# Kernel tuning notes

Hardware: AMD Instinct MI355X
Metric: run time of the kernel (lower is better)

The kernel has to match this reference:

```python
import jax, jax.numpy as jnp
import numpy as np

N_SAM, N_GEN, N_E = 10000, 20000, 1000000
D_SAM, D_GEN = 2000, 500
D0, H = 256, [256, 128, 64]
SLOPE = 0.25


def _glorot(key, shape):
    fan_in, fan_out = shape
    s = jnp.sqrt(2.0 / (fan_in + fan_out))
    return jax.random.normal(key, shape, dtype=jnp.float32) * s


def setup_inputs() -> dict:
    key = jax.random.key(0)
    ks = jax.random.split(key, 24)
    inp = {
        "sam_feat": jax.random.normal(ks[0], (N_SAM, D_SAM), dtype=jnp.float32),
        "gen_feat": jax.random.normal(ks[1], (N_GEN, D_GEN), dtype=jnp.float32),
        "src_sg": jax.random.randint(ks[2], (N_E,), 0, N_SAM, dtype=jnp.int32),
        "dst_sg": jax.random.randint(ks[3], (N_E,), 0, N_GEN, dtype=jnp.int32),
        "src_gs": jax.random.randint(ks[4], (N_E,), 0, N_GEN, dtype=jnp.int32),
        "dst_gs": jax.random.randint(ks[5], (N_E,), 0, N_SAM, dtype=jnp.int32),
        # input projections (LinearLayer, xavier init)
        "l1_W": _glorot(ks[6], (D_SAM, D0)), "l1_b": jnp.zeros((D0,), jnp.float32),
        "l2_W": _glorot(ks[7], (D_GEN, D0)), "l2_b": jnp.zeros((D0,), jnp.float32),
    }
    dims = [(D0, H[0]), (H[0], H[1]), (H[1], H[2])]
    k = 8
    for i, (di, do) in enumerate(dims, start=1):
        for rel in ("sg", "gs"):
            inp[f"W{i}_{rel}"] = _glorot(ks[k], (di, do)); k += 1
            inp[f"b{i}_{rel}"] = jnp.zeros((do,), jnp.float32)
    return inp


def _graph_conv(h_src, src, dst, n_src, n_dst, W, b):
    """DGL GraphConv with norm='both': D_dst^{-1/2} A D_src^{-1/2} h W + b."""
    ones = jnp.ones(src.shape, dtype=h_src.dtype)
    deg_out = jnp.clip(jax.ops.segment_sum(ones, src, num_segments=n_src), 1.0)
    deg_in = jnp.clip(jax.ops.segment_sum(ones, dst, num_segments=n_dst), 1.0)
    h = h_src * jax.lax.rsqrt(deg_out)[:, None]
    agg = jax.ops.segment_sum(h[src], dst, num_segments=n_dst)  # [n_dst, d]
    agg = agg * jax.lax.rsqrt(deg_in)[:, None]
    return agg @ W + b


def reference(sam_feat, gen_feat, src_sg, dst_sg, src_gs, dst_gs,
              l1_W, l1_b, l2_W, l2_b,
              W1_sg, b1_sg, W1_gs, b1_gs,
              W2_sg, b2_sg, W2_gs, b2_gs,
              W3_sg, b3_sg, W3_gs, b3_gs):
    h_sam = sam_feat @ l1_W + l1_b
    h_gen = gen_feat @ l2_W + l2_b
    layers = [(W1_sg, b1_sg, W1_gs, b1_gs),
              (W2_sg, b2_sg, W2_gs, b2_gs),
              (W3_sg, b3_sg, W3_gs, b3_gs)]
    for Wsg, bsg, Wgs, bgs in layers:
        # HeteroGraphConv(sum): dst 'gen' receives from sam_gen, dst 'sam' from gen_sam
        new_gen = _graph_conv(h_sam, src_sg, dst_sg, N_SAM, N_GEN, Wsg, bsg)
        new_sam = _graph_conv(h_gen, src_gs, dst_gs, N_GEN, N_SAM, Wgs, bgs)
        h_sam = jax.nn.leaky_relu(new_sam, SLOPE)  # dropout is identity in eval mode
        h_gen = jax.nn.leaky_relu(new_gen, SLOPE)
    return h_sam, h_gen
```

## Files before the change

### kernel.cpp

```cpp
#include <hip/hip_runtime.h>
#include <hip/hip_bf16.h>
#include <stdint.h>

#define N_SAM 10000
#define N_GEN 20000
#define DSAM  2000
#define DGEN  500
#define NB    32
#define NBNS  10240
#define SSPAN 2560
#define MP_SAM 10048
#define MP_GEN 20032

typedef __hip_bfloat16 bf16;
typedef short bf16x8 __attribute__((ext_vector_type(8)));
typedef float f32x4 __attribute__((ext_vector_type(4)));
typedef float f32x2 __attribute__((ext_vector_type(2)));

__device__ __forceinline__ float bfbits2f(unsigned short u) {
    unsigned v = ((unsigned)u) << 16;
    return __builtin_bit_cast(float, v);
}
__device__ __forceinline__ unsigned short f2bfbits(float f) {
    bf16 h = __float2bfloat16(f);
    return __builtin_bit_cast(unsigned short, h);
}
__device__ __forceinline__ unsigned packbf2(float lo, float hi) {
    return ((unsigned)f2bfbits(lo)) | (((unsigned)f2bfbits(hi)) << 16);
}
__device__ __forceinline__ f32x2 b2f2(unsigned x) {
    f32x2 r;
    r.x = __builtin_bit_cast(float, x << 16);
    r.y = __builtin_bit_cast(float, x & 0xffff0000u);
    return r;
}
__device__ __forceinline__ void addu2(uint4 u, f32x2* a) {
    a[0] += b2f2(u.x);
    a[1] += b2f2(u.y);
    a[2] += b2f2(u.z);
    a[3] += b2f2(u.w);
}
__device__ __forceinline__ void gload16(const unsigned short* g, unsigned short* l) {
    __builtin_amdgcn_global_load_lds(
        (const __attribute__((address_space(1))) void*)g,
        (__attribute__((address_space(3))) void*)l, 16, 0, 0);
}

__global__ __launch_bounds__(1024) void hist_count_kernel(
    const int* __restrict__ ssg, const int* __restrict__ dsg,
    const int* __restrict__ sgs, const int* __restrict__ dgs,
    unsigned* __restrict__ cs_ssg, unsigned* __restrict__ cs_dsg,
    unsigned* __restrict__ cs_sgs, unsigned* __restrict__ cs_dgs,
    int ne, int chunk) {
    __shared__ unsigned bins[NBNS];
    const int* arr; unsigned* counts; int lo, hi, nb;
    switch (blockIdx.y) {
        case 0:  arr = ssg; counts = cs_ssg; lo = 0;     hi = 10000; nb = 10000; break;
        case 1:  arr = dsg; counts = cs_dsg; lo = 0;     hi = 10240; nb = 20000; break;
        case 2:  arr = dsg; counts = cs_dsg; lo = 10240; hi = 20000; nb = 20000; break;
        case 3:  arr = sgs; counts = cs_sgs; lo = 0;     hi = 10240; nb = 20000; break;
        case 4:  arr = sgs; counts = cs_sgs; lo = 10240; hi = 20000; nb = 20000; break;
        default: arr = dgs; counts = cs_dgs; lo = 0;     hi = 10000; nb = 10000; break;
    }
    int span = hi - lo;
    for (int i = threadIdx.x; i < span; i += 1024) bins[i] = 0u;
    __syncthreads();
    int blk = blockIdx.x;
    int e0 = blk * chunk;
    int e1 = e0 + chunk; if (e1 > ne) e1 = ne;
    for (int e = e0 + threadIdx.x; e < e1; e += 1024) {
        int b = arr[e];
        if (b >= lo && b < hi) atomicAdd(&bins[b - lo], 1u);
    }
    __syncthreads();
    unsigned* out = counts + (size_t)blk * nb + lo;
    for (int i = threadIdx.x; i < span; i += 1024) out[i] = bins[i];
}

__global__ __launch_bounds__(256) void reduce_counts_kernel(
    const unsigned* __restrict__ cs_ssg, const unsigned* __restrict__ cs_dsg,
    const unsigned* __restrict__ cs_sgs, const unsigned* __restrict__ cs_dgs,
    unsigned* __restrict__ cnt_dsg, unsigned* __restrict__ cnt_dgs,
    float* __restrict__ rs_out_sam, float* __restrict__ rs_in_gen,
    float* __restrict__ rs_out_gen, float* __restrict__ rs_in_sam) {
    int i = blockIdx.x * 256 + threadIdx.x;
    int which = blockIdx.y;
    const unsigned* cs; int nb;
    switch (which) {
        case 0:  cs = cs_ssg; nb = 10000; break;
        case 1:  cs = cs_dsg; nb = 20000; break;
        case 2:  cs = cs_sgs; nb = 20000; break;
        default: cs = cs_dgs; nb = 10000; break;
    }
    if (i >= nb) return;
    unsigned s = 0;
    #pragma unroll 4
    for (int b = 0; b < NB; b++) s += cs[(size_t)b * nb + i];
    unsigned c = (s < 1u) ? 1u : s;
    float r = rsqrtf((float)c);
    if (which == 0)      { rs_out_sam[i] = r; }
    else if (which == 1) { cnt_dsg[i] = s; rs_in_gen[i] = r; }
    else if (which == 2) { rs_out_gen[i] = r; }
    else                 { cnt_dgs[i] = s; rs_in_sam[i] = r; }
}

__global__ __launch_bounds__(1024) void scan2_kernel(
    const unsigned* __restrict__ c0, unsigned* __restrict__ r0, int nA,
    const unsigned* __restrict__ c1, unsigned* __restrict__ r1, int nB) {
    const unsigned* cnt; unsigned* row; int n;
    if (blockIdx.x == 0) { cnt = c0; row = r0; n = nA; }
    else                 { cnt = c1; row = r1; n = nB; }
    __shared__ unsigned sdata[1024];
    __shared__ unsigned carry_s;
    int t = threadIdx.x;
    if (t == 0) carry_s = 0;
    __syncthreads();
    for (int base = 0; base < n; base += 1024) {
        int i = base + t;
        unsigned v = (i < n) ? cnt[i] : 0u;
        sdata[t] = v;
        __syncthreads();
        for (int off = 1; off < 1024; off <<= 1) {
            unsigned add = (t >= off) ? sdata[t - off] : 0u;
            __syncthreads();
            sdata[t] += add;
            __syncthreads();
        }
        unsigned incl = sdata[t];
        unsigned carry = carry_s;
        if (i < n) row[i] = carry + incl - v;
        __syncthreads();
        if (t == 1023) carry_s = carry + incl;
        __syncthreads();
    }
    if (t == 0) row[n] = carry_s;
}

__global__ __launch_bounds__(256) void cursor_kernel(
    const unsigned* __restrict__ cs_dsg, const unsigned* __restrict__ cs_dgs,
    const unsigned* __restrict__ row_sg, const unsigned* __restrict__ row_gs,
    unsigned* __restrict__ cur_sg_m, unsigned* __restrict__ cur_gs_m) {
    int i = blockIdx.x * 256 + threadIdx.x;
    const unsigned* cs; const unsigned* row; unsigned* cur; int nb;
    if (blockIdx.y == 0) { cs = cs_dsg; row = row_sg; cur = cur_sg_m; nb = 20000; }
    else                 { cs = cs_dgs; row = row_gs; cur = cur_gs_m; nb = 10000; }
    if (i >= nb) return;
    unsigned run = row[i];
    for (int b = 0; b < NB; b++) {
        cur[(size_t)b * nb + i] = run;
        run += cs[(size_t)b * nb + i];
    }
}

__global__ __launch_bounds__(1024) void scatter_sorted_kernel(
    const int* __restrict__ src_sg, const int* __restrict__ dst_sg,
    const int* __restrict__ src_gs, const int* __restrict__ dst_gs,
    const unsigned* __restrict__ cur_sg_m, const unsigned* __restrict__ cur_gs_m,
    int* __restrict__ col_sg, int* __restrict__ col_gs, int ne, int chunk) {
    __shared__ unsigned curs[SSPAN];
    int sl = blockIdx.y;
    const int* src; const int* dst; const unsigned* cmat; int* col; int lo, hi, nb;
    if (sl < 8) {
        src = src_sg; dst = dst_sg; cmat = cur_sg_m; col = col_sg; nb = 20000;
        lo = sl * SSPAN; hi = lo + SSPAN; if (hi > 20000) hi = 20000;
    } else {
        src = src_gs; dst = dst_gs; cmat = cur_gs_m; col = col_gs; nb = 10000;
        lo = (sl - 8) * SSPAN; hi = lo + SSPAN; if (hi > 10000) hi = 10000;
    }
    int span = hi - lo, blk = blockIdx.x;
    const unsigned* cin = cmat + (size_t)blk * nb + lo;
    for (int i = threadIdx.x; i < span; i += 1024) curs[i] = cin[i];
    __syncthreads();
    int e0 = blk * chunk;
    int e1 = e0 + chunk; if (e1 > ne) e1 = ne;
    for (int e = e0 + threadIdx.x; e < e1; e += 1024) {
        int d = dst[e];
        if (d >= lo && d < hi) {
            unsigned p = atomicAdd(&curs[d - lo], 1u);
            col[p] = src[e];
        }
    }
}

__global__ __launch_bounds__(256) void convert_feat_kernel(
    const float* __restrict__ src, unsigned short* __restrict__ dst,
    int M, int K, int Mp, int kshift) {
    const int Kp = 1 << kshift;
    size_t ng = ((size_t)Mp << kshift) >> 3;
    for (size_t gi = (size_t)blockIdx.x * 256 + threadIdx.x; gi < ng;
         gi += (size_t)gridDim.x * 256) {
        size_t o8 = gi << 3;
        int row = (int)(o8 >> kshift);
        int col = (int)(o8 & (size_t)(Kp - 1));
        uint4 out;
        if (row < M && col + 8 <= K) {
            const float* p = src + (size_t)row * K + col;
            float4 u0 = *reinterpret_cast<const float4*>(p);
            float4 u1 = *reinterpret_cast<const float4*>(p + 4);
            out.x = packbf2(u0.x, u0.y);
            out.y = packbf2(u0.z, u0.w);
            out.z = packbf2(u1.x, u1.y);
            out.w = packbf2(u1.z, u1.w);
        } else {
            unsigned short v[8];
            #pragma unroll
            for (int j = 0; j < 8; j++) {
                float f = 0.0f;
                if (row < M && col + j < K) f = src[(size_t)row * K + col + j];
                v[j] = f2bfbits(f);
            }
            out.x = ((unsigned)v[0]) | (((unsigned)v[1]) << 16);
            out.y = ((unsigned)v[2]) | (((unsigned)v[3]) << 16);
            out.z = ((unsigned)v[4]) | (((unsigned)v[5]) << 16);
            out.w = ((unsigned)v[6]) | (((unsigned)v[7]) << 16);
        }
        *reinterpret_cast<uint4*>(dst + o8) = out;
    }
}

__global__ __launch_bounds__(256) void zero_pad_kernel(
    unsigned short* __restrict__ p0, int n0,
    unsigned short* __restrict__ p1, int n1) {
    int i = blockIdx.x * 256 + threadIdx.x;
    if (i < n0) p0[i] = 0;
    if (i < n1) p1[i] = 0;
}

struct WDesc { const float* src; unsigned short* dst; int K, N, Kp; };
struct WPack { WDesc d[8]; };

__global__ __launch_bounds__(256) void transpose_weights_kernel(WPack p) {
    WDesc d = p.d[blockIdx.z];
    int n  = blockIdx.x * 32 + threadIdx.x;
    int kp = blockIdx.y * 8 + threadIdx.y;
    if (n >= d.N || kp >= d.Kp) return;
    float v = (kp < d.K) ? d.src[(size_t)kp * d.N + n] : 0.0f;
    d.dst[(size_t)n * d.Kp + kp] = f2bfbits(v);
}

struct GemmDesc {
    const unsigned short* A; const unsigned short* BT;
    const float* bias; const float* rs; unsigned short* C;
    int M, N, Kp, GX, GY;
};

__global__ __launch_bounds__(256) void gemm2_bf16(GemmDesc da, GemmDesc db, int nblkA) {
    int bi = blockIdx.x;
    GemmDesc d;
    if (bi < nblkA) { d = da; } else { d = db; bi -= nblkA; }
    int xcd = bi & 7, g = bi >> 3;
    int ntile = g % d.GX;
    int mtile = (g / d.GX) * 8 + xcd;
    if (mtile >= d.GY) return;
    int m0 = mtile * 64, n0 = ntile * 64;
    int Kp = d.Kp;

    __shared__ __attribute__((aligned(16))) unsigned short As[2][64 * 64];
    __shared__ __attribute__((aligned(16))) unsigned short Bs[2][64 * 64];

    int t = threadIdx.x;
    int lane = t & 63;
    int wave = t >> 6;
    int wm = (wave >> 1) * 32, wn = (wave & 1) * 32;
    int q = lane >> 4, mr = lane & 15;

    int r0 = t >> 3;
    int sw = ((t & 7) ^ (r0 & 7)) << 3;
    const unsigned short* a0 = d.A + (size_t)(m0 + r0) * Kp + sw;
    const unsigned short* b0 = d.BT + (size_t)(n0 + r0) * Kp + sw;
    const size_t rstep = (size_t)32 * Kp;
    unsigned short* asl0 = &As[0][t * 8];
    unsigned short* asl1 = &As[0][(256 + t) * 8];
    unsigned short* bsl0 = &Bs[0][t * 8];
    unsigned short* bsl1 = &Bs[0][(256 + t) * 8];
    const int bufoff = 64 * 64;

    f32x4 acc[2][2] = {};

    gload16(a0, asl0);
    gload16(a0 + rstep, asl1);
    gload16(b0, bsl0);
    gload16(b0 + rstep, bsl1);
    __syncthreads();

    int nt = Kp >> 6;
    for (int it = 0; it < nt; ++it) {
        int cur = it & 1;
        if (it + 1 < nt) {
            int k0 = (it + 1) << 6;
            int boff = (cur ^ 1) * bufoff;
            gload16(a0 + k0,         asl0 + boff);
            gload16(a0 + rstep + k0, asl1 + boff);
            gload16(b0 + k0,         bsl0 + boff);
            gload16(b0 + rstep + k0, bsl1 + boff);
        }
        #pragma unroll
        for (int kk = 0; kk < 64; kk += 32) {
            bf16x8 af[2], bfr[2];
            int cb = (kk >> 3) + q;
            #pragma unroll
            for (int i = 0; i < 2; i++) {
                int row = wm + i * 16 + mr;
                af[i] = *reinterpret_cast<const bf16x8*>(
                    &As[cur][row * 64 + ((cb ^ (row & 7)) << 3)]);
            }
            #pragma unroll
            for (int j = 0; j < 2; j++) {
                int row = wn + j * 16 + mr;
                bfr[j] = *reinterpret_cast<const bf16x8*>(
                    &Bs[cur][row * 64 + ((cb ^ (row & 7)) << 3)]);
            }
            #pragma unroll
            for (int i = 0; i < 2; i++)
                #pragma unroll
                for (int j = 0; j < 2; j++)
                    acc[i][j] = __builtin_amdgcn_mfma_f32_16x16x32_bf16(
                        af[i], bfr[j], acc[i][j], 0, 0, 0);
        }
        __syncthreads();
    }

    #pragma unroll
    for (int i = 0; i < 2; i++) {
        #pragma unroll
        for (int r = 0; r < 4; r++) {
            int row = m0 + wm + i * 16 + q * 4 + r;
            if (row >= d.M) continue;
            float sc = (d.rs != nullptr) ? d.rs[row] : 1.0f;
            #pragma unroll
            for (int j = 0; j < 2; j++) {
                int col = n0 + wn + j * 16 + mr;
                float v = acc[i][j][r];
                if (d.bias != nullptr) v += d.bias[col];
                v *= sc;
                d.C[(size_t)row * d.N + col] = f2bfbits(v);
            }
        }
    }
}

struct AggTask {
    const unsigned* rowptr; const int* col; const unsigned short* P;
    const float* rs_in; const float* bias; const float* rs_next;
    void* out;
    int row_begin; int row_end; int D; int d0; int lprs;
};
struct AggPack { AggTask t[8]; };

template <bool OUTBF>
__global__ __launch_bounds__(256) void agg_xcd_kernel(AggPack pk) {
    int task = blockIdx.x & 7;
    int lblk = blockIdx.x >> 3;
    int nlb  = (int)gridDim.x >> 3;
    AggTask t = pk.t[task];
    int lane = threadIdx.x & 63;
    int wav  = threadIdx.x >> 6;
    const int LPR = 1 << t.lprs;
    const int R   = 64 >> t.lprs;
    int sub = lane >> t.lprs;
    int li  = lane & (LPR - 1);
    const int D = t.D;
    const unsigned short* __restrict__ P = t.P + t.d0 + li * 8;
    const int* __restrict__ col = t.col;
    const int R4 = R << 2;

    for (int r = t.row_begin + lblk * 4 + wav; r < t.row_end; r += nlb * 4) {
        unsigned e0 = t.rowptr[r], e1 = t.rowptr[r + 1];
        f32x2 ac0[4] = {}, ac1[4] = {};
        unsigned e = e0;
        for (; e + (unsigned)R4 <= e1; e += R4) {
            int s0 = col[e + sub];
            int s1 = col[e + R + sub];
            int s2 = col[e + 2 * R + sub];
            int s3 = col[e + 3 * R + sub];
            uint4 u0 = *reinterpret_cast<const uint4*>(P + (size_t)s0 * D);
            uint4 u1 = *reinterpret_cast<const uint4*>(P + (size_t)s1 * D);
            uint4 u2 = *reinterpret_cast<const uint4*>(P + (size_t)s2 * D);
            uint4 u3 = *reinterpret_cast<const uint4*>(P + (size_t)s3 * D);
            addu2(u0, ac0); addu2(u1, ac1); addu2(u2, ac0); addu2(u3, ac1);
        }
        for (; e < e1; e += R) {
            unsigned idx = e + sub;
            if (idx < e1) {
                int s0 = col[idx];
                uint4 u = *reinterpret_cast<const uint4*>(P + (size_t)s0 * D);
                addu2(u, ac0);
            }
        }
        float acf[8];
        #pragma unroll
        for (int j = 0; j < 4; j++) {
            f32x2 s = ac0[j] + ac1[j];
            acf[2 * j]     = s.x;
            acf[2 * j + 1] = s.y;
        }
        for (int off = 32; off >= LPR; off >>= 1) {
            #pragma unroll
            for (int j = 0; j < 8; j++) acf[j] += __shfl_down(acf[j], off);
        }
        if (sub == 0) {
            float rsv = t.rs_in[r];
            float res[8];
            #pragma unroll
            for (int j = 0; j < 8; j++) {
                float v = acf[j] * rsv + t.bias[t.d0 + li * 8 + j];
                res[j] = (v >= 0.f) ? v : 0.25f * v;
            }
            if constexpr (OUTBF) {
                float sn = t.rs_next[r];
                uint4 o;
                o.x = packbf2(res[0] * sn, res[1] * sn);
                o.y = packbf2(res[2] * sn, res[3] * sn);
                o.z = packbf2(res[4] * sn, res[5] * sn);
                o.w = packbf2(res[6] * sn, res[7] * sn);
                *reinterpret_cast<uint4*>(
                    (unsigned short*)t.out + (size_t)r * D + t.d0 + li * 8) = o;
            } else {
                float* op = (float*)t.out + (size_t)r * D + t.d0 + li * 8;
                *reinterpret_cast<float4*>(op)     = make_float4(res[0], res[1], res[2], res[3]);
                *reinterpret_cast<float4*>(op + 4) = make_float4(res[4], res[5], res[6], res[7]);
            }
        }
    }
}

extern "C" void kernel_launch(void* const* d_in, const int* in_sizes, int n_in,
                              void* d_out, int out_size, void* d_ws, size_t ws_size,
                              hipStream_t stream) {
    const float* sam_feat = (const float*)d_in[0];
    const float* gen_feat = (const float*)d_in[1];
    const int* src_sg = (const int*)d_in[2];
    const int* dst_sg = (const int*)d_in[3];
    const int* src_gs = (const int*)d_in[4];
    const int* dst_gs = (const int*)d_in[5];
    const float* l1W = (const float*)d_in[6];
    const float* l1b = (const float*)d_in[7];
    const float* l2W = (const float*)d_in[8];
    const float* l2b = (const float*)d_in[9];
    const float* Wsg[3] = {(const float*)d_in[10], (const float*)d_in[14], (const float*)d_in[18]};
    const float* bsg[3] = {(const float*)d_in[11], (const float*)d_in[15], (const float*)d_in[19]};
    const float* Wgs[3] = {(const float*)d_in[12], (const float*)d_in[16], (const float*)d_in[20]};
    const float* bgs[3] = {(const float*)d_in[13], (const float*)d_in[17], (const float*)d_in[21]};
    const int NE = in_sizes[2];
    const int CHUNK = (NE + NB - 1) / NB;

    char* base = (char*)d_ws;
    size_t off = 0;
    auto alloc = [&](size_t bytes) -> char* {
        char* p = base + off;
        off = (off + bytes + 255) & ~(size_t)255;
        return p;
    };
    unsigned* cs_ssg = (unsigned*)alloc((size_t)NB * N_SAM * 4);
    unsigned* cs_dsg = (unsigned*)alloc((size_t)NB * N_GEN * 4);
    unsigned* cs_sgs = (unsigned*)alloc((size_t)NB * N_GEN * 4);
    unsigned* cs_dgs = (unsigned*)alloc((size_t)NB * N_SAM * 4);
    unsigned* cnt_dsg = (unsigned*)alloc(N_GEN * 4);
    unsigned* cnt_dgs = (unsigned*)alloc(N_SAM * 4);
    unsigned* row_sg = (unsigned*)alloc((N_GEN + 1) * 4);
    unsigned* row_gs = (unsigned*)alloc((N_SAM + 1) * 4);
    unsigned* cur_sg_m = (unsigned*)alloc((size_t)NB * N_GEN * 4);
    unsigned* cur_gs_m = (unsigned*)alloc((size_t)NB * N_SAM * 4);
    float* rs_out_sam = (float*)alloc(N_SAM * 4);
    float* rs_in_sam  = (float*)alloc(N_SAM * 4);
    float* rs_out_gen = (float*)alloc(N_GEN * 4);
    float* rs_in_gen  = (float*)alloc(N_GEN * 4);
    int* col_sg = (int*)alloc((size_t)NE * 4);
    int* col_gs = (int*)alloc((size_t)NE * 4);
    unsigned short* hs = (unsigned short*)alloc((size_t)MP_SAM * 256 * 2);
    unsigned short* hg = (unsigned short*)alloc((size_t)MP_GEN * 256 * 2);
    unsigned short* ps = (unsigned short*)alloc((size_t)N_SAM * 256 * 2);
    unsigned short* pg = (unsigned short*)alloc((size_t)N_GEN * 256 * 2);
    const int KP1 = 2048, KP2 = 512;
    unsigned short* BT_l1 = (unsigned short*)alloc((size_t)256 * KP1 * 2);
    unsigned short* BT_l2 = (unsigned short*)alloc((size_t)256 * KP2 * 2);
    unsigned short* BT_sg[3], *BT_gs[3];
    const int LN[3] = {256, 128, 64};
    const int LK[3] = {256, 256, 128};
    for (int i = 0; i < 3; i++) {
        BT_sg[i] = (unsigned short*)alloc((size_t)LN[i] * LK[i] * 2);
        BT_gs[i] = (unsigned short*)alloc((size_t)LN[i] * LK[i] * 2);
    }
    unsigned short* A_sam = (unsigned short*)alloc((size_t)MP_SAM * KP1 * 2);
    unsigned short* A_gen = (unsigned short*)alloc((size_t)MP_GEN * KP2 * 2);
    (void)ws_size;

    hist_count_kernel<<<dim3(NB, 6), 1024, 0, stream>>>(
        src_sg, dst_sg, src_gs, dst_gs, cs_ssg, cs_dsg, cs_sgs, cs_dgs, NE, CHUNK);
    reduce_counts_kernel<<<dim3((N_GEN + 255) / 256, 4), 256, 0, stream>>>(
        cs_ssg, cs_dsg, cs_sgs, cs_dgs, cnt_dsg, cnt_dgs,
        rs_out_sam, rs_in_gen, rs_out_gen, rs_in_sam);
    scan2_kernel<<<2, 1024, 0, stream>>>(cnt_dsg, row_sg, N_GEN, cnt_dgs, row_gs, N_SAM);
    cursor_kernel<<<dim3((N_GEN + 255) / 256, 2), 256, 0, stream>>>(
        cs_dsg, cs_dgs, row_sg, row_gs, cur_sg_m, cur_gs_m);
    scatter_sorted_kernel<<<dim3(NB, 12), 1024, 0, stream>>>(
        src_sg, dst_sg, src_gs, dst_gs, cur_sg_m, cur_gs_m, col_sg, col_gs, NE, CHUNK);

    convert_feat_kernel<<<2048, 256, 0, stream>>>(sam_feat, A_sam, N_SAM, DSAM, MP_SAM, 11);
    convert_feat_kernel<<<1024, 256, 0, stream>>>(gen_feat, A_gen, N_GEN, DGEN, MP_GEN, 9);
    zero_pad_kernel<<<48, 256, 0, stream>>>(
        hs + (size_t)N_SAM * 256, (MP_SAM - N_SAM) * 256,
        hg + (size_t)N_GEN * 256, (MP_GEN - N_GEN) * 256);

    WPack wp;
    wp.d[0] = {l1W,    BT_l1,    DSAM, 256, KP1};
    wp.d[1] = {l2W,    BT_l2,    DGEN, 256, KP2};
    wp.d[2] = {Wsg[0], BT_sg[0], 256, 256, 256};
    wp.d[3] = {Wgs[0], BT_gs[0], 256, 256, 256};
    wp.d[4] = {Wsg[1], BT_sg[1], 256, 128, 256};
    wp.d[5] = {Wgs[1], BT_gs[1], 256, 128, 256};
    wp.d[6] = {Wsg[2], BT_sg[2], 128, 64, 128};
    wp.d[7] = {Wgs[2], BT_gs[2], 128, 64, 128};
    transpose_weights_kernel<<<dim3(8, KP1 / 8, 8), dim3(32, 8), 0, stream>>>(wp);

    dim3 blk(256);
    const int GY_SAM = (N_SAM + 63) / 64;
    const int GY_GEN = (N_GEN + 63) / 64;
    auto swgrid = [](int GX, int GY) { return 8 * GX * ((GY + 7) / 8); };
    const int AGG_GRID = 2048;

    auto mkg = [](const unsigned short* A, const unsigned short* BT,
                  const float* bias, const float* rs, unsigned short* C,
                  int M, int N, int Kp, int GX, int GY) {
        GemmDesc d; d.A = A; d.BT = BT; d.bias = bias; d.rs = rs; d.C = C;
        d.M = M; d.N = N; d.Kp = Kp; d.GX = GX; d.GY = GY; return d;
    };
    auto mk = [](const unsigned* rp, const int* cl, const unsigned short* P,
                 const float* ri, const float* bi, const float* rn, void* out,
                 int rb, int re, int D, int d0, int lprs) {
        AggTask t; t.rowptr = rp; t.col = cl; t.P = P; t.rs_in = ri; t.bias = bi;
        t.rs_next = rn; t.out = out; t.row_begin = rb; t.row_end = re;
        t.D = D; t.d0 = d0; t.lprs = lprs; return t;
    };

    {
        int nA = swgrid(4, GY_SAM), nB = swgrid(4, GY_GEN);
        gemm2_bf16<<<nA + nB, blk, 0, stream>>>(
            mkg(A_sam, BT_l1, l1b, rs_out_sam, hs, N_SAM, 256, KP1, 4, GY_SAM),
            mkg(A_gen, BT_l2, l2b, rs_out_gen, hg, N_GEN, 256, KP2, 4, GY_GEN), nA);
    }

    {
        int nA = swgrid(4, GY_SAM), nB = swgrid(4, GY_GEN);
        gemm2_bf16<<<nA + nB, blk, 0, stream>>>(
            mkg(hs, BT_sg[0], nullptr, nullptr, ps, N_SAM, 256, 256, 4, GY_SAM),
            mkg(hg, BT_gs[0], nullptr, nullptr, pg, N_GEN, 256, 256, 4, GY_GEN), nA);
    }
    {
        AggPack p;
        p.t[0] = mk(row_sg, col_sg, ps, rs_in_gen, bsg[0], rs_out_gen, hg, 0, 10000, 256,   0, 4);
        p.t[1] = mk(row_sg, col_sg, ps, rs_in_gen, bsg[0], rs_out_gen, hg, 10000, 20000, 256, 0, 4);
        p.t[2] = mk(row_sg, col_sg, ps, rs_in_gen, bsg[0], rs_out_gen, hg, 0, 10000, 256, 128, 4);
        p.t[3] = mk(row_sg, col_sg, ps, rs_in_gen, bsg[0], rs_out_gen, hg, 10000, 20000, 256, 128, 4);
        p.t[4] = mk(row_gs, col_gs, pg, rs_in_sam, bgs[0], rs_out_sam, hs, 0, 10000, 256,   0, 3);
        p.t[5] = mk(row_gs, col_gs, pg, rs_in_sam, bgs[0], rs_out_sam, hs, 0, 10000, 256,  64, 3);
        p.t[6] = mk(row_gs, col_gs, pg, rs_in_sam, bgs[0], rs_out_sam, hs, 0, 10000, 256, 128, 3);
        p.t[7] = mk(row_gs, col_gs, pg, rs_in_sam, bgs[0], rs_out_sam, hs, 0, 10000, 256, 192, 3);
        agg_xcd_kernel<true><<<AGG_GRID, blk, 0, stream>>>(p);
    }

    {
        int nA = swgrid(2, GY_SAM), nB = swgrid(2, GY_GEN);
        gemm2_bf16<<<nA + nB, blk, 0, stream>>>(
            mkg(hs, BT_sg[1], nullptr, nullptr, ps, N_SAM, 128, 256, 2, GY_SAM),
            mkg(hg, BT_gs[1], nullptr, nullptr, pg, N_GEN, 128, 256, 2, GY_GEN), nA);
    }
    {
        AggPack p;
        p.t[0] = mk(row_sg, col_sg, ps, rs_in_gen, bsg[1], rs_out_gen, hg, 0, 5000, 128, 0, 4);
        p.t[1] = mk(row_sg, col_sg, ps, rs_in_gen, bsg[1], rs_out_gen, hg, 5000, 10000, 128, 0, 4);
        p.t[2] = mk(row_sg, col_sg, ps, rs_in_gen, bsg[1], rs_out_gen, hg, 10000, 15000, 128, 0, 4);
        p.t[3] = mk(row_sg, col_sg, ps, rs_in_gen, bsg[1], rs_out_gen, hg, 15000, 20000, 128, 0, 4);
        p.t[4] = mk(row_gs, col_gs, pg, rs_in_sam, bgs[1], rs_out_sam, hs, 0, 5000, 128,  0, 3);
        p.t[5] = mk(row_gs, col_gs, pg, rs_in_sam, bgs[1], rs_out_sam, hs, 5000, 10000, 128, 0, 3);
        p.t[6] = mk(row_gs, col_gs, pg, rs_in_sam, bgs[1], rs_out_sam, hs, 0, 5000, 128, 64, 3);
        p.t[7] = mk(row_gs, col_gs, pg, rs_in_sam, bgs[1], rs_out_sam, hs, 5000, 10000, 128, 64, 3);
        agg_xcd_kernel<true><<<AGG_GRID, blk, 0, stream>>>(p);
    }

    {
        int nA = swgrid(1, GY_SAM), nB = swgrid(1, GY_GEN);
        gemm2_bf16<<<nA + nB, blk, 0, stream>>>(
            mkg(hs, BT_sg[2], nullptr, nullptr, ps, N_SAM, 64, 128, 1, GY_SAM),
            mkg(hg, BT_gs[2], nullptr, nullptr, pg, N_GEN, 64, 128, 1, GY_GEN), nA);
    }
    float* out_sam = (float*)d_out;
    float* out_gen = out_sam + (size_t)N_SAM * 64;
    {
        AggPack p;
        p.t[0] = mk(row_sg, col_sg, ps, rs_in_gen, bsg[2], nullptr, out_gen, 0, 5000, 64, 0, 3);
        p.t[1] = mk(row_sg, col_sg, ps, rs_in_gen, bsg[2], nullptr, out_gen, 5000, 10000, 64, 0, 3);
        p.t[2] = mk(row_sg, col_sg, ps, rs_in_gen, bsg[2], nullptr, out_gen, 10000, 15000, 64, 0, 3);
        p.t[3] = mk(row_sg, col_sg, ps, rs_in_gen, bsg[2], nullptr, out_gen, 15000, 20000, 64, 0, 3);
        p.t[4] = mk(row_gs, col_gs, pg, rs_in_sam, bgs[2], nullptr, out_sam, 0, 2500, 64, 0, 3);
        p.t[5] = mk(row_gs, col_gs, pg, rs_in_sam, bgs[2], nullptr, out_sam, 2500, 5000, 64, 0, 3);
        p.t[6] = mk(row_gs, col_gs, pg, rs_in_sam, bgs[2], nullptr, out_sam, 5000, 7500, 64, 0, 3);
        p.t[7] = mk(row_gs, col_gs, pg, rs_in_sam, bgs[2], nullptr, out_sam, 7500, 10000, 64, 0, 3);
        agg_xcd_kernel<false><<<AGG_GRID, blk, 0, stream>>>(p);
    }
}
```

Measured before the change: 499.7 us.

## Fuse scan, feature conversion and padding into one launch; templatize aggregation

The serial two-block CSR prefix scan, both fp32-to-bf16 feature conversions and the zero-padding are merged into one kernel launch. The conversion blocks can now run alongside the slow single-block scans, and the change also removes launch overhead. The aggregation kernel is templated on feature width and lanes-per-row, so index math becomes compile-time constant, and it uses 32-bit offsets. The cost is a heavier combined kernel with 1024-thread blocks for the conversion, plus more template instantiations.

New measurement: 463.5 us. -7.3%, faster.

```diff
diff --git a/kernel.cpp b/kernel.cpp
--- a/kernel.cpp
+++ b/kernel.cpp
@@ -104,91 +104,22 @@
     else                 { cnt_dgs[i] = s; rs_in_sam[i] = r; }
 }
 
-__global__ __launch_bounds__(1024) void scan2_kernel(
-    const unsigned* __restrict__ c0, unsigned* __restrict__ r0, int nA,
-    const unsigned* __restrict__ c1, unsigned* __restrict__ r1, int nB) {
-    const unsigned* cnt; unsigned* row; int n;
-    if (blockIdx.x == 0) { cnt = c0; row = r0; n = nA; }
-    else                 { cnt = c1; row = r1; n = nB; }
-    __shared__ unsigned sdata[1024];
-    __shared__ unsigned carry_s;
-    int t = threadIdx.x;
-    if (t == 0) carry_s = 0;
-    __syncthreads();
-    for (int base = 0; base < n; base += 1024) {
-        int i = base + t;
-        unsigned v = (i < n) ? cnt[i] : 0u;
-        sdata[t] = v;
-        __syncthreads();
-        for (int off = 1; off < 1024; off <<= 1) {
-            unsigned add = (t >= off) ? sdata[t - off] : 0u;
-            __syncthreads();
-            sdata[t] += add;
-            __syncthreads();
-        }
-        unsigned incl = sdata[t];
-        unsigned carry = carry_s;
-        if (i < n) row[i] = carry + incl - v;
-        __syncthreads();
-        if (t == 1023) carry_s = carry + incl;
-        __syncthreads();
-    }
-    if (t == 0) row[n] = carry_s;
-}
-
-__global__ __launch_bounds__(256) void cursor_kernel(
-    const unsigned* __restrict__ cs_dsg, const unsigned* __restrict__ cs_dgs,
-    const unsigned* __restrict__ row_sg, const unsigned* __restrict__ row_gs,
-    unsigned* __restrict__ cur_sg_m, unsigned* __restrict__ cur_gs_m) {
-    int i = blockIdx.x * 256 + threadIdx.x;
-    const unsigned* cs; const unsigned* row; unsigned* cur; int nb;
-    if (blockIdx.y == 0) { cs = cs_dsg; row = row_sg; cur = cur_sg_m; nb = 20000; }
-    else                 { cs = cs_dgs; row = row_gs; cur = cur_gs_m; nb = 10000; }
-    if (i >= nb) return;
-    unsigned run = row[i];
-    for (int b = 0; b < NB; b++) {
-        cur[(size_t)b * nb + i] = run;
-        run += cs[(size_t)b * nb + i];
-    }
-}
-
-__global__ __launch_bounds__(1024) void scatter_sorted_kernel(
-    const int* __restrict__ src_sg, const int* __restrict__ dst_sg,
-    const int* __restrict__ src_gs, const int* __restrict__ dst_gs,
-    const unsigned* __restrict__ cur_sg_m, const unsigned* __restrict__ cur_gs_m,
-    int* __restrict__ col_sg, int* __restrict__ col_gs, int ne, int chunk) {
-    __shared__ unsigned curs[SSPAN];
-    int sl = blockIdx.y;
-    const int* src; const int* dst; const unsigned* cmat; int* col; int lo, hi, nb;
-    if (sl < 8) {
-        src = src_sg; dst = dst_sg; cmat = cur_sg_m; col = col_sg; nb = 20000;
-        lo = sl * SSPAN; hi = lo + SSPAN; if (hi > 20000) hi = 20000;
-    } else {
-        src = src_gs; dst = dst_gs; cmat = cur_gs_m; col = col_gs; nb = 10000;
-        lo = (sl - 8) * SSPAN; hi = lo + SSPAN; if (hi > 10000) hi = 10000;
-    }
-    int span = hi - lo, blk = blockIdx.x;
-    const unsigned* cin = cmat + (size_t)blk * nb + lo;
-    for (int i = threadIdx.x; i < span; i += 1024) curs[i] = cin[i];
-    __syncthreads();
-    int e0 = blk * chunk;
-    int e1 = e0 + chunk; if (e1 > ne) e1 = ne;
-    for (int e = e0 + threadIdx.x; e < e1; e += 1024) {
-        int d = dst[e];
-        if (d >= lo && d < hi) {
-            unsigned p = atomicAdd(&curs[d - lo], 1u);
-            col[p] = src[e];
-        }
-    }
-}
-
-__global__ __launch_bounds__(256) void convert_feat_kernel(
+struct ScanConvArgs {
+    const unsigned* c0; unsigned* r0; int nA;
+    const unsigned* c1; unsigned* r1; int nB;
+    const float* fsrcA; unsigned short* fdstA;
+    const float* fsrcB; unsigned short* fdstB;
+    unsigned short* z0; int nz0; unsigned short* z1; int nz1;
+    int nConvA, nConvB;
+};
+
+__device__ __forceinline__ void conv_body(
     const float* __restrict__ src, unsigned short* __restrict__ dst,
-    int M, int K, int Mp, int kshift) {
+    int M, int K, int Mp, int kshift, int cb, int ncb) {
     const int Kp = 1 << kshift;
     size_t ng = ((size_t)Mp << kshift) >> 3;
-    for (size_t gi = (size_t)blockIdx.x * 256 + threadIdx.x; gi < ng;
-         gi += (size_t)gridDim.x * 256) {
+    for (size_t gi = (size_t)cb * 1024 + threadIdx.x; gi < ng;
+         gi += (size_t)ncb * 1024) {
         size_t o8 = gi << 3;
         int row = (int)(o8 >> kshift);
         int col = (int)(o8 & (size_t)(Kp - 1));
@@ -218,12 +149,92 @@
     }
 }
 
-__global__ __launch_bounds__(256) void zero_pad_kernel(
-    unsigned short* __restrict__ p0, int n0,
-    unsigned short* __restrict__ p1, int n1) {
+__global__ __launch_bounds__(1024) void scan_conv_kernel(ScanConvArgs a) {
+    int b = blockIdx.x;
+    if (b < 2) {
+        const unsigned* cnt; unsigned* row; int n;
+        if (b == 0) { cnt = a.c0; row = a.r0; n = a.nA; }
+        else        { cnt = a.c1; row = a.r1; n = a.nB; }
+        __shared__ unsigned sdata[1024];
+        __shared__ unsigned carry_s;
+        int t = threadIdx.x;
+        if (t == 0) carry_s = 0;
+        __syncthreads();
+        for (int base = 0; base < n; base += 1024) {
+            int i = base + t;
+            unsigned v = (i < n) ? cnt[i] : 0u;
+            sdata[t] = v;
+            __syncthreads();
+            for (int off = 1; off < 1024; off <<= 1) {
+                unsigned add = (t >= off) ? sdata[t - off] : 0u;
+                __syncthreads();
+                sdata[t] += add;
+                __syncthreads();
+            }
+            unsigned incl = sdata[t];
+            unsigned carry = carry_s;
+            if (i < n) row[i] = carry + incl - v;
+            __syncthreads();
+            if (t == 1023) carry_s = carry + incl;
+            __syncthreads();
+        }
+        if (t == 0) row[n] = carry_s;
+    } else if (b < 2 + a.nConvA) {
+        conv_body(a.fsrcA, a.fdstA, N_SAM, DSAM, MP_SAM, 11, b - 2, a.nConvA);
+    } else if (b < 2 + a.nConvA + a.nConvB) {
+        conv_body(a.fsrcB, a.fdstB, N_GEN, DGEN, MP_GEN, 9,
+                  b - 2 - a.nConvA, a.nConvB);
+    } else {
+        int zb = b - 2 - a.nConvA - a.nConvB;
+        for (int i = zb * 1024 + threadIdx.x; i < a.nz0; i += 8 * 1024) a.z0[i] = 0;
+        for (int i = zb * 1024 + threadIdx.x; i < a.nz1; i += 8 * 1024) a.z1[i] = 0;
+    }
+}
+
+__global__ __launch_bounds__(256) void cursor_kernel(
+    const unsigned* __restrict__ cs_dsg, const unsigned* __restrict__ cs_dgs,
+    const unsigned* __restrict__ row_sg, const unsigned* __restrict__ row_gs,
+    unsigned* __restrict__ cur_sg_m, unsigned* __restrict__ cur_gs_m) {
     int i = blockIdx.x * 256 + threadIdx.x;
-    if (i < n0) p0[i] = 0;
-    if (i < n1) p1[i] = 0;
+    const unsigned* cs; const unsigned* row; unsigned* cur; int nb;
+    if (blockIdx.y == 0) { cs = cs_dsg; row = row_sg; cur = cur_sg_m; nb = 20000; }
+    else                 { cs = cs_dgs; row = row_gs; cur = cur_gs_m; nb = 10000; }
+    if (i >= nb) return;
+    unsigned run = row[i];
+    for (int b = 0; b < NB; b++) {
+        cur[(size_t)b * nb + i] = run;
+        run += cs[(size_t)b * nb + i];
+    }
+}
+
+__global__ __launch_bounds__(1024) void scatter_sorted_kernel(
+    const int* __restrict__ src_sg, const int* __restrict__ dst_sg,
+    const int* __restrict__ src_gs, const int* __restrict__ dst_gs,
+    const unsigned* __restrict__ cur_sg_m, const unsigned* __restrict__ cur_gs_m,
+    int* __restrict__ col_sg, int* __restrict__ col_gs, int ne, int chunk) {
+    __shared__ unsigned curs[SSPAN];
+    int sl = blockIdx.y;
+    const int* src; const int* dst; const unsigned* cmat; int* col; int lo, hi, nb;
+    if (sl < 8) {
+        src = src_sg; dst = dst_sg; cmat = cur_sg_m; col = col_sg; nb = 20000;
+        lo = sl * SSPAN; hi = lo + SSPAN; if (hi > 20000) hi = 20000;
+    } else {
+        src = src_gs; dst = dst_gs; cmat = cur_gs_m; col = col_gs; nb = 10000;
+        lo = (sl - 8) * SSPAN; hi = lo + SSPAN; if (hi > 10000) hi = 10000;
+    }
+    int span = hi - lo, blk = blockIdx.x;
+    const unsigned* cin = cmat + (size_t)blk * nb + lo;
+    for (int i = threadIdx.x; i < span; i += 1024) curs[i] = cin[i];
+    __syncthreads();
+    int e0 = blk * chunk;
+    int e1 = e0 + chunk; if (e1 > ne) e1 = ne;
+    for (int e = e0 + threadIdx.x; e < e1; e += 1024) {
+        int d = dst[e];
+        if (d >= lo && d < hi) {
+            unsigned p = atomicAdd(&curs[d - lo], 1u);
+            col[p] = src[e];
+        }
+    }
 }
 
 struct WDesc { const float* src; unsigned short* dst; int K, N, Kp; };
@@ -343,47 +354,43 @@
     const unsigned* rowptr; const int* col; const unsigned short* P;
     const float* rs_in; const float* bias; const float* rs_next;
     void* out;
-    int row_begin; int row_end; int D; int d0; int lprs;
+    int row_begin; int row_end; int d0;
 };
 struct AggPack { AggTask t[8]; };
 
-template <bool OUTBF>
-__global__ __launch_bounds__(256) void agg_xcd_kernel(AggPack pk) {
-    int task = blockIdx.x & 7;
-    int lblk = blockIdx.x >> 3;
-    int nlb  = (int)gridDim.x >> 3;
-    AggTask t = pk.t[task];
+template <int D, int LPRS, bool OUTBF>
+__device__ __forceinline__ void agg_body(const AggTask& t, int lblk, int nlb) {
+    const int LPR = 1 << LPRS;
+    const int R   = 64 >> LPRS;
+    const int R4  = R * 4;
     int lane = threadIdx.x & 63;
     int wav  = threadIdx.x >> 6;
-    const int LPR = 1 << t.lprs;
-    const int R   = 64 >> t.lprs;
-    int sub = lane >> t.lprs;
+    int sub = lane >> LPRS;
     int li  = lane & (LPR - 1);
-    const int D = t.D;
-    const unsigned short* __restrict__ P = t.P + t.d0 + li * 8;
+    const unsigned li8 = (unsigned)li * 8;
+    const unsigned short* __restrict__ Pu = t.P + t.d0;
     const int* __restrict__ col = t.col;
-    const int R4 = R << 2;
 
     for (int r = t.row_begin + lblk * 4 + wav; r < t.row_end; r += nlb * 4) {
         unsigned e0 = t.rowptr[r], e1 = t.rowptr[r + 1];
         f32x2 ac0[4] = {}, ac1[4] = {};
         unsigned e = e0;
         for (; e + (unsigned)R4 <= e1; e += R4) {
-            int s0 = col[e + sub];
-            int s1 = col[e + R + sub];
-            int s2 = col[e + 2 * R + sub];
-            int s3 = col[e + 3 * R + sub];
-            uint4 u0 = *reinterpret_cast<const uint4*>(P + (size_t)s0 * D);
-            uint4 u1 = *reinterpret_cast<const uint4*>(P + (size_t)s1 * D);
-            uint4 u2 = *reinterpret_cast<const uint4*>(P + (size_t)s2 * D);
-            uint4 u3 = *reinterpret_cast<const uint4*>(P + (size_t)s3 * D);
+            unsigned s0 = (unsigned)col[e + sub];
+            unsigned s1 = (unsigned)col[e + R + sub];
+            unsigned s2 = (unsigned)col[e + 2 * R + sub];
+            unsigned s3 = (unsigned)col[e + 3 * R + sub];
+            uint4 u0 = *reinterpret_cast<const uint4*>(Pu + (s0 * (unsigned)D + li8));
+            uint4 u1 = *reinterpret_cast<const uint4*>(Pu + (s1 * (unsigned)D + li8));
+            uint4 u2 = *reinterpret_cast<const uint4*>(Pu + (s2 * (unsigned)D + li8));
+            uint4 u3 = *reinterpret_cast<const uint4*>(Pu + (s3 * (unsigned)D + li8));
             addu2(u0, ac0); addu2(u1, ac1); addu2(u2, ac0); addu2(u3, ac1);
         }
         for (; e < e1; e += R) {
             unsigned idx = e + sub;
             if (idx < e1) {
-                int s0 = col[idx];
-                uint4 u = *reinterpret_cast<const uint4*>(P + (size_t)s0 * D);
+                unsigned s0 = (unsigned)col[idx];
+                uint4 u = *reinterpret_cast<const uint4*>(Pu + (s0 * (unsigned)D + li8));
                 addu2(u, ac0);
             }
         }
@@ -394,6 +401,7 @@
             acf[2 * j]     = s.x;
             acf[2 * j + 1] = s.y;
         }
+        #pragma unroll
         for (int off = 32; off >= LPR; off >>= 1) {
             #pragma unroll
             for (int j = 0; j < 8; j++) acf[j] += __shfl_down(acf[j], off);
@@ -422,6 +430,15 @@
             }
         }
     }
+}
+
+template <int DG, int LGS, int DS, int LSS, bool OUTBF>
+__global__ __launch_bounds__(256) void agg_xcd_kernel(AggPack pk) {
+    int task = blockIdx.x & 7;
+    int lblk = blockIdx.x >> 3;
+    int nlb  = (int)gridDim.x >> 3;
+    if (task < 4) agg_body<DG, LGS, OUTBF>(pk.t[task], lblk, nlb);
+    else          agg_body<DS, LSS, OUTBF>(pk.t[task], lblk, nlb);
 }
 
 extern "C" void kernel_launch(void* const* d_in, const int* in_sizes, int n_in,
@@ -490,17 +507,23 @@
     reduce_counts_kernel<<<dim3((N_GEN + 255) / 256, 4), 256, 0, stream>>>(
         cs_ssg, cs_dsg, cs_sgs, cs_dgs, cnt_dsg, cnt_dgs,
         rs_out_sam, rs_in_gen, rs_out_gen, rs_in_sam);
-    scan2_kernel<<<2, 1024, 0, stream>>>(cnt_dsg, row_sg, N_GEN, cnt_dgs, row_gs, N_SAM);
+
+    {
+        ScanConvArgs a;
+        a.c0 = cnt_dsg; a.r0 = row_sg; a.nA = N_GEN;
+        a.c1 = cnt_dgs; a.r1 = row_gs; a.nB = N_SAM;
+        a.fsrcA = sam_feat; a.fdstA = A_sam;
+        a.fsrcB = gen_feat; a.fdstB = A_gen;
+        a.z0 = hs + (size_t)N_SAM * 256; a.nz0 = (MP_SAM - N_SAM) * 256;
+        a.z1 = hg + (size_t)N_GEN * 256; a.nz1 = (MP_GEN - N_GEN) * 256;
+        a.nConvA = 1536; a.nConvB = 768;
+        scan_conv_kernel<<<2 + 1536 + 768 + 8, 1024, 0, stream>>>(a);
+    }
+
     cursor_kernel<<<dim3((N_GEN + 255) / 256, 2), 256, 0, stream>>>(
         cs_dsg, cs_dgs, row_sg, row_gs, cur_sg_m, cur_gs_m);
     scatter_sorted_kernel<<<dim3(NB, 12), 1024, 0, stream>>>(
         src_sg, dst_sg, src_gs, dst_gs, cur_sg_m, cur_gs_m, col_sg, col_gs, NE, CHUNK);
-
-    convert_feat_kernel<<<2048, 256, 0, stream>>>(sam_feat, A_sam, N_SAM, DSAM, MP_SAM, 11);
-    convert_feat_kernel<<<1024, 256, 0, stream>>>(gen_feat, A_gen, N_GEN, DGEN, MP_GEN, 9);
-    zero_pad_kernel<<<48, 256, 0, stream>>>(
-        hs + (size_t)N_SAM * 256, (MP_SAM - N_SAM) * 256,
-        hg + (size_t)N_GEN * 256, (MP_GEN - N_GEN) * 256);
 
     WPack wp;
     wp.d[0] = {l1W,    BT_l1,    DSAM, 256, KP1};
@@ -527,10 +550,10 @@
     };
     auto mk = [](const unsigned* rp, const int* cl, const unsigned short* P,
                  const float* ri, const float* bi, const float* rn, void* out,
-                 int rb, int re, int D, int d0, int lprs) {
+                 int rb, int re, int d0) {
         AggTask t; t.rowptr = rp; t.col = cl; t.P = P; t.rs_in = ri; t.bias = bi;
         t.rs_next = rn; t.out = out; t.row_begin = rb; t.row_end = re;
-        t.D = D; t.d0 = d0; t.lprs = lprs; return t;
+        t.d0 = d0; return t;
     };
 
     {
@@ -548,15 +571,15 @@
     }
     {
         AggPack p;
-        p.t[0] = mk(row_sg, col_sg, ps, rs_in_gen, bsg[0], rs_out_gen, hg, 0, 10000, 256,   0, 4);
-        p.t[1] = mk(row_sg, col_sg, ps, rs_in_gen, bsg[0], rs_out_gen, hg, 10000, 20000, 256, 0, 4);
-        p.t[2] = mk(row_sg, col_sg, ps, rs_in_gen, bsg[0], rs_out_gen, hg, 0, 10000, 256, 128, 4);
-        p.t[3] = mk(row_sg, col_sg, ps, rs_in_gen, bsg[0], rs_out_gen, hg, 10000, 20000, 256, 128, 4);
-        p.t[4] = mk(row_gs, col_gs, pg, rs_in_sam, bgs[0], rs_out_sam, hs, 0, 10000, 256,   0, 3);
-        p.t[5] = mk(row_gs, col_gs, pg, rs_in_sam, bgs[0], rs_out_sam, hs, 0, 10000, 256,  64, 3);
-        p.t[6] = mk(row_gs, col_gs, pg, rs_in_sam, bgs[0], rs_out_sam, hs, 0, 10000, 256, 128, 3);
-        p.t[7] = mk(row_gs, col_gs, pg, rs_in_sam, bgs[0], rs_out_sam, hs, 0, 10000, 256, 192, 3);
-        agg_xcd_kernel<true><<<AGG_GRID, blk, 0, stream>>>(p);
+        p.t[0] = mk(row_sg, col_sg, ps, rs_in_gen, bsg[0], rs_out_gen, hg, 0, 10000,   0);
+        p.t[1] = mk(row_sg, col_sg, ps, rs_in_gen, bsg[0], rs_out_gen, hg, 10000, 20000, 0);
+        p.t[2] = mk(row_sg, col_sg, ps, rs_in_gen, bsg[0], rs_out_gen, hg, 0, 10000, 128);
+        p.t[3] = mk(row_sg, col_sg, ps, rs_in_gen, bsg[0], rs_out_gen, hg, 10000, 20000, 128);
+        p.t[4] = mk(row_gs, col_gs, pg, rs_in_sam, bgs[0], rs_out_sam, hs, 0, 10000,   0);
+        p.t[5] = mk(row_gs, col_gs, pg, rs_in_sam, bgs[0], rs_out_sam, hs, 0, 10000,  64);
+        p.t[6] = mk(row_gs, col_gs, pg, rs_in_sam, bgs[0], rs_out_sam, hs, 0, 10000, 128);
+        p.t[7] = mk(row_gs, col_gs, pg, rs_in_sam, bgs[0], rs_out_sam, hs, 0, 10000, 192);
+        agg_xcd_kernel<256, 4, 256, 3, true><<<AGG_GRID, blk, 0, stream>>>(p);
     }
 
     {
@@ -567,15 +590,15 @@
     }
     {
         AggPack p;
-        p.t[0] = mk(row_sg, col_sg, ps, rs_in_gen, bsg[1], rs_out_gen, hg, 0, 5000, 128, 0, 4);
-        p.t[1] = mk(row_sg, col_sg, ps, rs_in_gen, bsg[1], rs_out_gen, hg, 5000, 10000, 128, 0, 4);
-        p.t[2] = mk(row_sg, col_sg, ps, rs_in_gen, bsg[1], rs_out_gen, hg, 10000, 15000, 128, 0, 4);
-        p.t[3] = mk(row_sg, col_sg, ps, rs_in_gen, bsg[1], rs_out_gen, hg, 15000, 20000, 128, 0, 4);
-        p.t[4] = mk(row_gs, col_gs, pg, rs_in_sam, bgs[1], rs_out_sam, hs, 0, 5000, 128,  0, 3);
-        p.t[5] = mk(row_gs, col_gs, pg, rs_in_sam, bgs[1], rs_out_sam, hs, 5000, 10000, 128, 0, 3);
-        p.t[6] = mk(row_gs, col_gs, pg, rs_in_sam, bgs[1], rs_out_sam, hs, 0, 5000, 128, 64, 3);
-        p.t[7] = mk(row_gs, col_gs, pg, rs_in_sam, bgs[1], rs_out_sam, hs, 5000, 10000, 128, 64, 3);
-        agg_xcd_kernel<true><<<AGG_GRID, blk, 0, stream>>>(p);
+        p.t[0] = mk(row_sg, col_sg, ps, rs_in_gen, bsg[1], rs_out_gen, hg, 0, 5000, 0);
+        p.t[1] = mk(row_sg, col_sg, ps, rs_in_gen, bsg[1], rs_out_gen, hg, 5000, 10000, 0);
+        p.t[2] = mk(row_sg, col_sg, ps, rs_in_gen, bsg[1], rs_out_gen, hg, 10000, 15000, 0);
+        p.t[3] = mk(row_sg, col_sg, ps, rs_in_gen, bsg[1], rs_out_gen, hg, 15000, 20000, 0);
+        p.t[4] = mk(row_gs, col_gs, pg, rs_in_sam, bgs[1], rs_out_sam, hs, 0, 5000,  0);
+        p.t[5] = mk(row_gs, col_gs, pg, rs_in_sam, bgs[1], rs_out_sam, hs, 5000, 10000, 0);
+        p.t[6] = mk(row_gs, col_gs, pg, rs_in_sam, bgs[1], rs_out_sam, hs, 0, 5000, 64);
+        p.t[7] = mk(row_gs, col_gs, pg, rs_in_sam, bgs[1], rs_out_sam, hs, 5000, 10000, 64);
+        agg_xcd_kernel<128, 4, 128, 3, true><<<AGG_GRID, blk, 0, stream>>>(p);
     }
 
     {
@@ -588,14 +611,14 @@
     float* out_gen = out_sam + (size_t)N_SAM * 64;
     {
         AggPack p;
-        p.t[0] = mk(row_sg, col_sg, ps, rs_in_gen, bsg[2], nullptr, out_gen, 0, 5000, 64, 0, 3);
-        p.t[1] = mk(row_sg, col_sg, ps, rs_in_gen, bsg[2], nullptr, out_gen, 5000, 10000, 64, 0, 3);
-        p.t[2] = mk(row_sg, col_sg, ps, rs_in_gen, bsg[2], nullptr, out_gen, 10000, 15000, 64, 0, 3);
-        p.t[3] = mk(row_sg, col_sg, ps, rs_in_gen, bsg[2], nullptr, out_gen, 15000, 20000, 64, 0, 3);
-        p.t[4] = mk(row_gs, col_gs, pg, rs_in_sam, bgs[2], nullptr, out_sam, 0, 2500, 64, 0, 3);
-        p.t[5] = mk(row_gs, col_gs, pg, rs_in_sam, bgs[2], nullptr, out_sam, 2500, 5000, 64, 0, 3);
-        p.t[6] = mk(row_gs, col_gs, pg, rs_in_sam, bgs[2], nullptr, out_sam, 5000, 7500, 64, 0, 3);
-        p.t[7] = mk(row_gs, col_gs, pg, rs_in_sam, bgs[2], nullptr, out_sam, 7500, 10000, 64, 0, 3);
-        agg_xcd_kernel<false><<<AGG_GRID, blk, 0, stream>>>(p);
-    }
-}
+        p.t[0] = mk(row_sg, col_sg, ps, rs_in_gen, bsg[2], nullptr, out_gen, 0, 5000, 0);
+        p.t[1] = mk(row_sg, col_sg, ps, rs_in_gen, bsg[2], nullptr, out_gen, 5000, 10000, 0);
+        p.t[2] = mk(row_sg, col_sg, ps, rs_in_gen, bsg[2], nullptr, out_gen, 10000, 15000, 0);
+        p.t[3] = mk(row_sg, col_sg, ps, rs_in_gen, bsg[2], nullptr, out_gen, 15000, 20000, 0);
+        p.t[4] = mk(row_gs, col_gs, pg, rs_in_sam, bgs[2], nullptr, out_sam, 0, 2500, 0);
+        p.t[5] = mk(row_gs, col_gs, pg, rs_in_sam, bgs[2], nullptr, out_sam, 2500, 5000, 0);
+        p.t[6] = mk(row_gs, col_gs, pg, rs_in_sam, bgs[2], nullptr, out_sam, 5000, 7500, 0);
+        p.t[7] = mk(row_gs, col_gs, pg, rs_in_sam, bgs[2], nullptr, out_sam, 7500, 10000, 0);
+        agg_xcd_kernel<64, 3, 64, 3, false><<<AGG_GRID, blk, 0, stream>>>(p);
+    }
+}
```
